# Kernel tuning notes

Measured on AMD Instinct MI355X. Metric: run time of the kernel, lower is better.

The kernel has to match this reference:

```python
import jax, jax.numpy as jnp
import numpy as np

B, N, D, H = 4, 2048, 1024, 16
DH = D // H

def setup_inputs() -> dict:
    key = jax.random.key(0)
    kx, kqkv, ko = jax.random.split(key, 3)
    x = jax.random.normal(kx, (B, N, D), dtype=jnp.float32)
    # torch Linear weights: [out, in]; scale like default init
    W_qkv = jax.random.normal(kqkv, (3 * D, D), dtype=jnp.float32) * (1.0 / np.sqrt(D))
    W_out = jax.random.normal(ko, (D, D), dtype=jnp.float32) * (1.0 / np.sqrt(D))
    return {"x": x, "W_qkv": W_qkv, "W_out": W_out}

def reference(x, W_qkv, W_out):
    Bk, Nk, C = x.shape
    qkv = jnp.einsum('bnc,oc->bno', x, W_qkv)  # [B,N,3D]
    qkv = qkv.reshape(Bk, Nk, 3, H, DH).transpose(2, 0, 3, 1, 4)  # [3,B,H,N,DH]
    q, k, v = qkv[0], qkv[1], qkv[2]
    att = jnp.einsum('bhnd,bhmd->bhnm', q, k) * (1.0 / np.sqrt(DH))
    mask = jnp.triu(jnp.ones((Nk, Nk), dtype=bool), k=1)  # True above diagonal
    att = jnp.where(mask, -jnp.inf, att)
    att = jax.nn.softmax(att, axis=-1)
    y = jnp.einsum('bhnm,bhmd->bhnd', att, v)  # [B,H,N,DH]
    y = y.transpose(0, 2, 1, 3).reshape(Bk, Nk, C)
    return jnp.einsum('bnc,oc->bno', y, W_out)
```

## Files before the change

### kernel.cpp

```cpp
#include <hip/hip_runtime.h>
#include <hip/hip_bf16.h>
#include <stdint.h>

#define Bb 4
#define Nn 2048
#define Dd 1024
#define Hh 16
#define DHd 64
#define Mm (Bb*Nn)
#define D3 (3*Dd)

typedef unsigned short u16;
typedef unsigned int u32;
typedef __attribute__((ext_vector_type(8))) short bf16x8;
typedef __attribute__((ext_vector_type(4))) float f32x4;
typedef __attribute__((ext_vector_type(2))) unsigned int u32x2;
typedef __attribute__((ext_vector_type(4))) unsigned int u32x4;

__device__ __forceinline__ u16 f2bf(float f) {
    unsigned int u = __float_as_uint(f);
    u = (u + 0x7FFFu + ((u >> 16) & 1u)) >> 16;
    return (u16)u;
}

__device__ __forceinline__ u32 cvtpk_bf16(float lo, float hi) {
    u32 r;
    asm("v_cvt_pk_bf16_f32 %0, %1, %2" : "=v"(r) : "v"(lo), "v"(hi));
    return r;
}

__device__ __forceinline__ float fexp2(float x) {
    float r;
    asm("v_exp_f32 %0, %1" : "=v"(r) : "v"(x));
    return r;
}

#define GLOAD16(g, l)                                                          \
    __builtin_amdgcn_global_load_lds(                                          \
        (const __attribute__((address_space(1))) unsigned int*)(g),            \
        (__attribute__((address_space(3))) unsigned int*)(l), 16, 0, 0)

__global__ void cvt_f32_bf16(const float* __restrict__ in, u16* __restrict__ out, int n4) {
    int i = blockIdx.x * blockDim.x + threadIdx.x;
    int stride = gridDim.x * blockDim.x;
    for (; i < n4; i += stride) {
        float4 v = ((const float4*)in)[i];
        u16 o0 = f2bf(v.x), o1 = f2bf(v.y), o2 = f2bf(v.z), o3 = f2bf(v.w);
        unsigned int lo = (unsigned int)o0 | ((unsigned int)o1 << 16);
        unsigned int hi = (unsigned int)o2 | ((unsigned int)o3 << 16);
        ((uint2*)out)[i] = make_uint2(lo, hi);
    }
}

__global__ void cvt_f32_bf16_s(const float* __restrict__ in, u16* __restrict__ out,
                               int n4, int cut4, float s) {
    int i = blockIdx.x * blockDim.x + threadIdx.x;
    int stride = gridDim.x * blockDim.x;
    for (; i < n4; i += stride) {
        float4 v = ((const float4*)in)[i];
        float sc = (i < cut4) ? s : 1.0f;
        u16 o0 = f2bf(v.x * sc), o1 = f2bf(v.y * sc), o2 = f2bf(v.z * sc), o3 = f2bf(v.w * sc);
        unsigned int lo = (unsigned int)o0 | ((unsigned int)o1 << 16);
        unsigned int hi = (unsigned int)o2 | ((unsigned int)o3 << 16);
        ((uint2*)out)[i] = make_uint2(lo, hi);
    }
}

template<int OUT_F32>
__global__ __launch_bounds__(256) void gemm_bt(const u16* __restrict__ A,
                                               const u16* __restrict__ Bm,
                                               void* __restrict__ C,
                                               int M, int Nout, int K) {
    __shared__ u16 As[128 * 64];
    __shared__ u16 Bs[128 * 64];
    const int t = threadIdx.x;
    const int lane = t & 63;
    const int w = t >> 6;
    const int wr = w >> 1, wc = w & 1;
    const int l15 = lane & 15, l4 = lane >> 4;
    const int m0 = blockIdx.y * 128;
    const int n0 = blockIdx.x * 128;

    f32x4 acc[4][4] = {};

    for (int k0 = 0; k0 < K; k0 += 64) {
        __syncthreads();
#pragma unroll
        for (int i = 0; i < 4; i++) {
            int chunk = i * 256 + t;
            int row = chunk >> 3;
            int csw = ((chunk & 7) ^ (row & 7)) << 3;
            GLOAD16(A + (size_t)(m0 + row) * K + k0 + csw, &As[chunk * 8]);
            GLOAD16(Bm + (size_t)(n0 + row) * K + k0 + csw, &Bs[chunk * 8]);
        }
        __syncthreads();

#pragma unroll
        for (int kh = 0; kh < 2; kh++) {
            bf16x8 a[4], b[4];
#pragma unroll
            for (int mi = 0; mi < 4; mi++) {
                int row = wr * 64 + mi * 16 + l15;
                a[mi] = *(const bf16x8*)&As[row * 64 + (((kh * 4 + l4) ^ (row & 7)) << 3)];
            }
#pragma unroll
            for (int nj = 0; nj < 4; nj++) {
                int row = wc * 64 + nj * 16 + l15;
                b[nj] = *(const bf16x8*)&Bs[row * 64 + (((kh * 4 + l4) ^ (row & 7)) << 3)];
            }
#pragma unroll
            for (int mi = 0; mi < 4; mi++)
#pragma unroll
                for (int nj = 0; nj < 4; nj++)
                    acc[mi][nj] = __builtin_amdgcn_mfma_f32_16x16x32_bf16(a[mi], b[nj], acc[mi][nj], 0, 0, 0);
        }
    }

#pragma unroll
    for (int mi = 0; mi < 4; mi++) {
#pragma unroll
        for (int nj = 0; nj < 4; nj++) {
            int col = n0 + wc * 64 + nj * 16 + l15;
#pragma unroll
            for (int r = 0; r < 4; r++) {
                int row = m0 + wr * 64 + mi * 16 + l4 * 4 + r;
                float v = acc[mi][nj][r];
                if (OUT_F32)
                    ((float*)C)[(size_t)row * Nout + col] = v;
                else
                    ((u16*)C)[(size_t)row * Nout + col] = f2bf(v);
            }
        }
    }
}

__global__ __launch_bounds__(512) void attn(const u16* __restrict__ qkv, u16* __restrict__ y) {
    __shared__ u16 Kt[2][64 * 64];
    __shared__ u16 Vt[2][64 * 64];

    const int t = threadIdx.x;
    const int lane = t & 63;
    const int w = t >> 6;
    const int l15 = lane & 15, l4 = lane >> 4;
    const int bh = blockIdx.x * 8 + (blockIdx.y & 7);
    const int pairidx = blockIdx.y >> 3;
    const int b = bh >> 4, h = bh & 15;

    const u16* qbase = qkv + (size_t)(b * Nn) * D3 + h * DHd;
    const u16* Kg = qbase + Dd;
    const u16* Vg = qbase + 2 * Dd;

    const int krow = t >> 3;
    const int ksw = (((t & 7) ^ (krow & 7)) << 3);
    const int vi = t & 31;
    const int vsd = (t >> 5) * 4;
    const int vchunk = (2 * vi) >> 3;
    const int vcol = (2 * vi) & 7;

    const bool hi2 = (lane >> 5) & 1;
    const bool bit0 = (lane >> 4) & 1;
    const int sgrp = lane & 48;

    bool mgt[4];
#pragma unroll
    for (int r = 0; r < 4; r++) mgt[r] = (l4 * 4 + r) > l15;

    for (int pass = 0; pass < 2; ++pass) {
        const int qt = pass == 0 ? pairidx : (15 - pairidx);
        const int q0 = qt * 128;
        const int ktmax = 2 * qt + 1;
        const int qwmin = q0 + w * 16;

        bf16x8 qf[2];
        {
            const u16* qrow = qbase + (size_t)(qwmin + l15) * D3;
            qf[0] = *(const bf16x8*)(qrow + l4 * 8);
            qf[1] = *(const bf16x8*)(qrow + 32 + l4 * 8);
        }

        f32x4 o[4] = {};
        float m_ = -1e30f;
        float l_ = 0.f;

        u32x2 va, vb_;

        GLOAD16(Kg + (size_t)krow * D3 + ksw, &Kt[0][t * 8]);
        {
            const u16* vr = Vg + (size_t)(2 * vi) * D3 + vsd;
            va = *(const u32x2*)vr;
            vb_ = *(const u32x2*)(vr + D3);
        }
        asm volatile("s_waitcnt vmcnt(0)" ::: "memory");
        {
            u16 av[4], bv[4];
            *(u32x2*)av = va; *(u32x2*)bv = vb_;
#pragma unroll
            for (int j = 0; j < 4; j++) {
                int d = vsd + j;
                u32 word = (u32)av[j] | ((u32)bv[j] << 16);
                *(u32*)&Vt[0][d * 64 + ((vchunk ^ (d & 7)) << 3) + vcol] = word;
            }
        }
        __syncthreads();

        int cur = 0;
        for (int kt = 0; kt <= ktmax; ++kt) {
            const int k0 = kt * 64;
            const int havenext = (kt < ktmax);

            if (havenext) {
                const int nk0 = k0 + 64;
                GLOAD16(Kg + (size_t)(nk0 + krow) * D3 + ksw, &Kt[cur ^ 1][t * 8]);
                const u16* vr = Vg + (size_t)(nk0 + 2 * vi) * D3 + vsd;
                va = *(const u32x2*)vr;
                vb_ = *(const u32x2*)(vr + D3);
            }

            const int dks = (qwmin - k0) >> 4;

            if (dks >= 0) {
                const int kcm = dks < 3 ? dks : 3;
                const int kgm = (dks >> 1) < 1 ? (dks >> 1) : 1;

                f32x4 sv[4];
                float vmax = -3.0e38f;
                __builtin_amdgcn_s_setprio(1);
#pragma unroll
                for (int kc = 0; kc < 4; ++kc) {
                    if (kc <= kcm) {
                        f32x4 s = {};
                        int row = kc * 16 + l15;
                        int sw = row & 7;
                        bf16x8 kf0 = *(const bf16x8*)&Kt[cur][row * 64 + ((l4 ^ sw) << 3)];
                        bf16x8 kf1 = *(const bf16x8*)&Kt[cur][row * 64 + (((4 + l4) ^ sw) << 3)];
                        s = __builtin_amdgcn_mfma_f32_16x16x32_bf16(kf0, qf[0], s, 0, 0, 0);
                        s = __builtin_amdgcn_mfma_f32_16x16x32_bf16(kf1, qf[1], s, 0, 0, 0);
                        const bool bmask = (kc == dks);
#pragma unroll
                        for (int r = 0; r < 4; r++) {
                            float x = s[r];
                            if (bmask && mgt[r]) x = -1e30f;
                            sv[kc][r] = x;
                            vmax = fmaxf(vmax, x);
                        }
                    }
                }
                __builtin_amdgcn_s_setprio(0);

                vmax = fmaxf(vmax, __shfl_xor(vmax, 16));
                vmax = fmaxf(vmax, __shfl_xor(vmax, 32));

                if (!__all(vmax <= m_ + 8.f)) {
                    float newm = fmaxf(m_, vmax);
                    float corr = fexp2(m_ - newm);
                    l_ *= corr;
                    float corr_o[4];
#pragma unroll
                    for (int r = 0; r < 4; ++r)
                        corr_o[r] = __shfl(corr, sgrp | (((lane >> 4) & 3) * 4 + r));
#pragma unroll
                    for (int db = 0; db < 4; db++)
#pragma unroll
                        for (int r = 0; r < 4; r++) o[db][r] *= corr_o[r];
                    m_ = newm;
                }

                u32 up[4][2];
#pragma unroll
                for (int kc = 0; kc < 4; ++kc) {
                    if (kc <= kcm) {
                        float p0 = fexp2(sv[kc][0] - m_);
                        float p1 = fexp2(sv[kc][1] - m_);
                        float p2 = fexp2(sv[kc][2] - m_);
                        float p3 = fexp2(sv[kc][3] - m_);
                        l_ += (p0 + p1) + (p2 + p3);
                        up[kc][0] = cvtpk_bf16(p0, p1);
                        up[kc][1] = cvtpk_bf16(p2, p3);
                    } else {
                        up[kc][0] = 0u;
                        up[kc][1] = 0u;
                    }
                }

                __builtin_amdgcn_s_setprio(1);
#pragma unroll
                for (int kg = 0; kg < 2; kg++) {
                    if (kg <= kgm) {
                        u32 paya0 = hi2 ? up[2 * kg + 1][0] : up[2 * kg][0];
                        u32 paya1 = hi2 ? up[2 * kg + 1][1] : up[2 * kg][1];
                        u32 payb0 = hi2 ? up[2 * kg][0] : up[2 * kg + 1][0];
                        u32 payb1 = hi2 ? up[2 * kg][1] : up[2 * kg + 1][1];
                        u32 a16_0 = (u32)__shfl_xor((int)paya0, 16);
                        u32 a16_1 = (u32)__shfl_xor((int)paya1, 16);
                        u32 a32_0 = (u32)__shfl_xor((int)payb0, 32);
                        u32 a32_1 = (u32)__shfl_xor((int)payb1, 32);
                        u32 a48_0 = (u32)__shfl_xor((int)payb0, 48);
                        u32 a48_1 = (u32)__shfl_xor((int)payb1, 48);
                        u32x4 tt;
                        tt[0] = hi2 ? (bit0 ? a16_0 : a32_0) : (bit0 ? a48_0 : paya0);
                        tt[1] = hi2 ? (bit0 ? a16_1 : a32_1) : (bit0 ? a48_1 : paya1);
                        tt[2] = hi2 ? (bit0 ? paya0 : a48_0) : (bit0 ? a32_0 : a16_0);
                        tt[3] = hi2 ? (bit0 ? paya1 : a48_1) : (bit0 ? a32_1 : a16_1);
                        union { u32x4 u; bf16x8 b; } pa;
                        pa.u = tt;
#pragma unroll
                        for (int db = 0; db < 4; db++) {
                            int d = db * 16 + l15;
                            bf16x8 vb = *(const bf16x8*)&Vt[cur][d * 64 + (((kg * 4 + l4) ^ (d & 7)) << 3)];
                            o[db] = __builtin_amdgcn_mfma_f32_16x16x32_bf16(pa.b, vb, o[db], 0, 0, 0);
                        }
                    }
                }
                __builtin_amdgcn_s_setprio(0);
            }

            if (havenext) {
                asm volatile("s_waitcnt vmcnt(0)" ::: "memory");
                u16 av[4], bv[4];
                *(u32x2*)av = va; *(u32x2*)bv = vb_;
#pragma unroll
                for (int j = 0; j < 4; j++) {
                    int d = vsd + j;
                    u32 word = (u32)av[j] | ((u32)bv[j] << 16);
                    *(u32*)&Vt[cur ^ 1][d * 64 + ((vchunk ^ (d & 7)) << 3) + vcol] = word;
                }
            }
            __syncthreads();
            cur ^= 1;
        }

        l_ += __shfl_xor(l_, 16);
        l_ += __shfl_xor(l_, 32);
        float linv = 1.f / l_;
        float linv_o[4];
#pragma unroll
        for (int r = 0; r < 4; ++r)
            linv_o[r] = __shfl(linv, sgrp | (((lane >> 4) & 3) * 4 + r));
#pragma unroll
        for (int r = 0; r < 4; r++) {
            int qg = qwmin + l4 * 4 + r;
            u16* yrow = y + (size_t)(b * Nn + qg) * Dd + h * DHd;
#pragma unroll
            for (int db = 0; db < 4; db++)
                yrow[db * 16 + l15] = f2bf(o[db][r] * linv_o[r]);
        }
    }
}

extern "C" void kernel_launch(void* const* d_in, const int* in_sizes, int n_in,
                              void* d_out, int out_size, void* d_ws, size_t ws_size,
                              hipStream_t stream) {
    const float* x = (const float*)d_in[0];
    const float* Wqkv = (const float*)d_in[1];
    const float* Wout = (const float*)d_in[2];

    char* ws = (char*)d_ws;
    size_t off = 0;
    u16* xb = (u16*)(ws + off);    off += (size_t)Mm * Dd * 2;
    u16* wqkvb = (u16*)(ws + off); off += (size_t)D3 * Dd * 2;
    u16* woutb = (u16*)(ws + off); off += (size_t)Dd * Dd * 2;
    u16* qkv = (u16*)(ws + off);   off += (size_t)Mm * D3 * 2;
    u16* yb = (u16*)(ws + off);    off += (size_t)Mm * Dd * 2;

    const float SCL = 0.125f * 1.4426950408889634f;

    cvt_f32_bf16<<<4096, 256, 0, stream>>>(x, xb, Mm * Dd / 4);
    cvt_f32_bf16_s<<<1024, 256, 0, stream>>>(Wqkv, wqkvb, D3 * Dd / 4, Dd * Dd / 4, SCL);
    cvt_f32_bf16<<<512, 256, 0, stream>>>(Wout, woutb, Dd * Dd / 4);

    gemm_bt<0><<<dim3(D3 / 128, Mm / 128), 256, 0, stream>>>(xb, wqkvb, qkv, Mm, D3, Dd);
    attn<<<dim3(Nn / 256, Bb * Hh), 512, 0, stream>>>(qkv, yb);
    gemm_bt<1><<<dim3(Dd / 128, Mm / 128), 256, 0, stream>>>(yb, woutb, d_out, Mm, Dd, Dd);
}
```

Baseline: 178.4 us.

## Split attention KV tiles across two wave groups and merge softmax partials in LDS

The attention block grows to 1024 threads, split into two groups of 8 waves. Each group processes alternating K/V tiles for the same query rows, giving a split-K flash-attention scheme whose partial max, sum and output are merged through shared memory at the end. Loading is also specialised: the first group issues K global-to-LDS loads and the second loads and transposes V. The aim is more parallelism per query tile. The cost is a larger LDS pool, register pressure from launch_bounds(1024,2), extra barriers and a merge step.

```diff
diff --git a/kernel.cpp b/kernel.cpp
--- a/kernel.cpp
+++ b/kernel.cpp
@@ -134,13 +134,19 @@
     }
 }
 
-__global__ __launch_bounds__(512) void attn(const u16* __restrict__ qkv, u16* __restrict__ y) {
-    __shared__ u16 Kt[2][64 * 64];
-    __shared__ u16 Vt[2][64 * 64];
+__global__ __launch_bounds__(1024, 2) void attn(const u16* __restrict__ qkv, u16* __restrict__ y) {
+    __shared__ __align__(16) char pool[35328];
+    u16 (*Kt)[4096] = reinterpret_cast<u16(*)[4096]>(pool);
+    u16 (*Vt)[4096] = reinterpret_cast<u16(*)[4096]>(pool + 16384);
+    float* MO = (float*)pool;
+    float* ML = (float*)(pool + 32768);
+    float* MM = (float*)(pool + 34816);
 
     const int t = threadIdx.x;
     const int lane = t & 63;
     const int w = t >> 6;
+    const int wl = w & 7;
+    const int par = w >> 3;
     const int l15 = lane & 15, l4 = lane >> 4;
     const int bh = blockIdx.x * 8 + (blockIdx.y & 7);
     const int pairidx = blockIdx.y >> 3;
@@ -152,8 +158,9 @@
 
     const int krow = t >> 3;
     const int ksw = (((t & 7) ^ (krow & 7)) << 3);
-    const int vi = t & 31;
-    const int vsd = (t >> 5) * 4;
+    const int tv = t & 511;
+    const int vi = tv & 31;
+    const int vsd = (tv >> 5) * 4;
     const int vchunk = (2 * vi) >> 3;
     const int vcol = (2 * vi) & 7;
 
@@ -169,7 +176,7 @@
         const int qt = pass == 0 ? pairidx : (15 - pairidx);
         const int q0 = qt * 128;
         const int ktmax = 2 * qt + 1;
-        const int qwmin = q0 + w * 16;
+        const int qwmin = q0 + wl * 16;
 
         bf16x8 qf[2];
         {
@@ -184,14 +191,13 @@
 
         u32x2 va, vb_;
 
-        GLOAD16(Kg + (size_t)krow * D3 + ksw, &Kt[0][t * 8]);
-        {
+        if (w < 8) {
+            GLOAD16(Kg + (size_t)krow * D3 + ksw, &Kt[0][t * 8]);
+        } else {
             const u16* vr = Vg + (size_t)(2 * vi) * D3 + vsd;
             va = *(const u32x2*)vr;
             vb_ = *(const u32x2*)(vr + D3);
-        }
-        asm volatile("s_waitcnt vmcnt(0)" ::: "memory");
-        {
+            asm volatile("s_waitcnt vmcnt(0)" ::: "memory");
             u16 av[4], bv[4];
             *(u32x2*)av = va; *(u32x2*)bv = vb_;
 #pragma unroll
@@ -210,15 +216,18 @@
 
             if (havenext) {
                 const int nk0 = k0 + 64;
-                GLOAD16(Kg + (size_t)(nk0 + krow) * D3 + ksw, &Kt[cur ^ 1][t * 8]);
-                const u16* vr = Vg + (size_t)(nk0 + 2 * vi) * D3 + vsd;
-                va = *(const u32x2*)vr;
-                vb_ = *(const u32x2*)(vr + D3);
+                if (w < 8) {
+                    GLOAD16(Kg + (size_t)(nk0 + krow) * D3 + ksw, &Kt[cur ^ 1][t * 8]);
+                } else {
+                    const u16* vr = Vg + (size_t)(nk0 + 2 * vi) * D3 + vsd;
+                    va = *(const u32x2*)vr;
+                    vb_ = *(const u32x2*)(vr + D3);
+                }
             }
 
             const int dks = (qwmin - k0) >> 4;
 
-            if (dks >= 0) {
+            if (((kt & 1) == par) && dks >= 0) {
                 const int kcm = dks < 3 ? dks : 3;
                 const int kgm = (dks >> 1) < 1 ? (dks >> 1) : 1;
 
@@ -314,7 +323,7 @@
                 __builtin_amdgcn_s_setprio(0);
             }
 
-            if (havenext) {
+            if (havenext && w >= 8) {
                 asm volatile("s_waitcnt vmcnt(0)" ::: "memory");
                 u16 av[4], bv[4];
                 *(u32x2*)av = va; *(u32x2*)bv = vb_;
@@ -329,21 +338,55 @@
             cur ^= 1;
         }
 
-        l_ += __shfl_xor(l_, 16);
-        l_ += __shfl_xor(l_, 32);
-        float linv = 1.f / l_;
-        float linv_o[4];
-#pragma unroll
-        for (int r = 0; r < 4; ++r)
-            linv_o[r] = __shfl(linv, sgrp | (((lane >> 4) & 3) * 4 + r));
-#pragma unroll
-        for (int r = 0; r < 4; r++) {
-            int qg = qwmin + l4 * 4 + r;
-            u16* yrow = y + (size_t)(b * Nn + qg) * Dd + h * DHd;
+        if (w >= 8) {
+            const int wu = w - 8;
+            if (lane < 16) MM[wu * 16 + lane] = m_;
+            ML[wu * 64 + lane] = l_;
+            float* mo = MO + wu * 1024 + lane * 16;
 #pragma unroll
             for (int db = 0; db < 4; db++)
-                yrow[db * 16 + l15] = f2bf(o[db][r] * linv_o[r]);
-        }
+                *(f32x4*)(mo + db * 4) = o[db];
+        }
+        __syncthreads();
+        if (w < 8) {
+            float mB = MM[wl * 16 + l15];
+            float M = fmaxf(m_, mB);
+            float ca = fexp2(m_ - M);
+            float cb = fexp2(mB - M);
+            l_ = l_ * ca + ML[wl * 64 + lane] * cb;
+            float ca_o[4], cb_o[4];
+#pragma unroll
+            for (int r = 0; r < 4; ++r) {
+                int src = sgrp | (((lane >> 4) & 3) * 4 + r);
+                ca_o[r] = __shfl(ca, src);
+                cb_o[r] = __shfl(cb, src);
+            }
+            const float* mo = MO + wl * 1024 + lane * 16;
+#pragma unroll
+            for (int db = 0; db < 4; db++) {
+                f32x4 ob = *(const f32x4*)(mo + db * 4);
+#pragma unroll
+                for (int r = 0; r < 4; r++)
+                    o[db][r] = o[db][r] * ca_o[r] + ob[r] * cb_o[r];
+            }
+
+            l_ += __shfl_xor(l_, 16);
+            l_ += __shfl_xor(l_, 32);
+            float linv = 1.f / l_;
+            float linv_o[4];
+#pragma unroll
+            for (int r = 0; r < 4; ++r)
+                linv_o[r] = __shfl(linv, sgrp | (((lane >> 4) & 3) * 4 + r));
+#pragma unroll
+            for (int r = 0; r < 4; r++) {
+                int qg = qwmin + l4 * 4 + r;
+                u16* yrow = y + (size_t)(b * Nn + qg) * Dd + h * DHd;
+#pragma unroll
+                for (int db = 0; db < 4; db++)
+                    yrow[db * 16 + l15] = f2bf(o[db][r] * linv_o[r]);
+            }
+        }
+        __syncthreads();
     }
 }
 
@@ -369,6 +412,6 @@
     cvt_f32_bf16<<<512, 256, 0, stream>>>(Wout, woutb, Dd * Dd / 4);
 
     gemm_bt<0><<<dim3(D3 / 128, Mm / 128), 256, 0, stream>>>(xb, wqkvb, qkv, Mm, D3, Dd);
-    attn<<<dim3(Nn / 256, Bb * Hh), 512, 0, stream>>>(qkv, yb);
+    attn<<<dim3(Nn / 256, Bb * Hh), 1024, 0, stream>>>(qkv, yb);
     gemm_bt<1><<<dim3(Dd / 128, Mm / 128), 256, 0, stream>>>(yb, woutb, d_out, Mm, Dd, Dd);
 }
```

Result: slower. 210.2 us (+17.8%).

## Shrink attention blocks to 64-row query tiles and swizzle GEMM tile order

Applied to the files above, without the earlier changes.

The attention kernel moves from 512-thread blocks handling 128-row query tiles to 256-thread blocks handling 64-row tiles. Each thread now loads twice as much K/V data, the grid grows to 8x128, and the diagonal-skip branch is removed because every warp now sees valid keys. The GEMM remaps block indices so groups of eight consecutive blocks land on strided tiles, aiming for better cache locality across XCDs. The goal is finer causal load balancing and higher occupancy, at the cost of more blocks reloading K/V overall.

```diff
diff --git a/kernel.cpp b/kernel.cpp
--- a/kernel.cpp
+++ b/kernel.cpp
@@ -14,7 +14,6 @@
 typedef unsigned int u32;
 typedef __attribute__((ext_vector_type(8))) short bf16x8;
 typedef __attribute__((ext_vector_type(4))) float f32x4;
-typedef __attribute__((ext_vector_type(2))) unsigned int u32x2;
 typedef __attribute__((ext_vector_type(4))) unsigned int u32x4;
 
 __device__ __forceinline__ u16 f2bf(float f) {
@@ -78,8 +77,13 @@
     const int w = t >> 6;
     const int wr = w >> 1, wc = w & 1;
     const int l15 = lane & 15, l4 = lane >> 4;
-    const int m0 = blockIdx.y * 128;
-    const int n0 = blockIdx.x * 128;
+
+    const int gx = gridDim.x;
+    const int linear = blockIdx.y * gx + blockIdx.x;
+    const int cpx = (gx * gridDim.y) >> 3;
+    const int tile = (linear & 7) * cpx + (linear >> 3);
+    const int m0 = (tile / gx) * 128;
+    const int n0 = (tile % gx) * 128;
 
     f32x4 acc[4][4] = {};
 
@@ -134,7 +138,7 @@
     }
 }
 
-__global__ __launch_bounds__(512) void attn(const u16* __restrict__ qkv, u16* __restrict__ y) {
+__global__ __launch_bounds__(256, 4) void attn(const u16* __restrict__ qkv, u16* __restrict__ y) {
     __shared__ u16 Kt[2][64 * 64];
     __shared__ u16 Vt[2][64 * 64];
 
@@ -153,7 +157,7 @@
     const int krow = t >> 3;
     const int ksw = (((t & 7) ^ (krow & 7)) << 3);
     const int vi = t & 31;
-    const int vsd = (t >> 5) * 4;
+    const int vsd = (t >> 5) * 8;
     const int vchunk = (2 * vi) >> 3;
     const int vcol = (2 * vi) & 7;
 
@@ -166,9 +170,9 @@
     for (int r = 0; r < 4; r++) mgt[r] = (l4 * 4 + r) > l15;
 
     for (int pass = 0; pass < 2; ++pass) {
-        const int qt = pass == 0 ? pairidx : (15 - pairidx);
-        const int q0 = qt * 128;
-        const int ktmax = 2 * qt + 1;
+        const int qt = pass == 0 ? pairidx : (31 - pairidx);
+        const int q0 = qt * 64;
+        const int ktmax = qt;
         const int qwmin = q0 + w * 16;
 
         bf16x8 qf[2];
@@ -182,20 +186,21 @@
         float m_ = -1e30f;
         float l_ = 0.f;
 
-        u32x2 va, vb_;
+        u32x4 va, vb_;
 
         GLOAD16(Kg + (size_t)krow * D3 + ksw, &Kt[0][t * 8]);
+        GLOAD16(Kg + (size_t)(krow + 32) * D3 + ksw, &Kt[0][(t + 256) * 8]);
         {
             const u16* vr = Vg + (size_t)(2 * vi) * D3 + vsd;
-            va = *(const u32x2*)vr;
-            vb_ = *(const u32x2*)(vr + D3);
+            va = *(const u32x4*)vr;
+            vb_ = *(const u32x4*)(vr + D3);
         }
         asm volatile("s_waitcnt vmcnt(0)" ::: "memory");
         {
-            u16 av[4], bv[4];
-            *(u32x2*)av = va; *(u32x2*)bv = vb_;
-#pragma unroll
-            for (int j = 0; j < 4; j++) {
+            u16 av[8], bv[8];
+            *(u32x4*)av = va; *(u32x4*)bv = vb_;
+#pragma unroll
+            for (int j = 0; j < 8; j++) {
                 int d = vsd + j;
                 u32 word = (u32)av[j] | ((u32)bv[j] << 16);
                 *(u32*)&Vt[0][d * 64 + ((vchunk ^ (d & 7)) << 3) + vcol] = word;
@@ -211,115 +216,113 @@
             if (havenext) {
                 const int nk0 = k0 + 64;
                 GLOAD16(Kg + (size_t)(nk0 + krow) * D3 + ksw, &Kt[cur ^ 1][t * 8]);
+                GLOAD16(Kg + (size_t)(nk0 + krow + 32) * D3 + ksw, &Kt[cur ^ 1][(t + 256) * 8]);
                 const u16* vr = Vg + (size_t)(nk0 + 2 * vi) * D3 + vsd;
-                va = *(const u32x2*)vr;
-                vb_ = *(const u32x2*)(vr + D3);
+                va = *(const u32x4*)vr;
+                vb_ = *(const u32x4*)(vr + D3);
             }
 
             const int dks = (qwmin - k0) >> 4;
-
-            if (dks >= 0) {
-                const int kcm = dks < 3 ? dks : 3;
-                const int kgm = (dks >> 1) < 1 ? (dks >> 1) : 1;
-
-                f32x4 sv[4];
-                float vmax = -3.0e38f;
-                __builtin_amdgcn_s_setprio(1);
-#pragma unroll
-                for (int kc = 0; kc < 4; ++kc) {
-                    if (kc <= kcm) {
-                        f32x4 s = {};
-                        int row = kc * 16 + l15;
-                        int sw = row & 7;
-                        bf16x8 kf0 = *(const bf16x8*)&Kt[cur][row * 64 + ((l4 ^ sw) << 3)];
-                        bf16x8 kf1 = *(const bf16x8*)&Kt[cur][row * 64 + (((4 + l4) ^ sw) << 3)];
-                        s = __builtin_amdgcn_mfma_f32_16x16x32_bf16(kf0, qf[0], s, 0, 0, 0);
-                        s = __builtin_amdgcn_mfma_f32_16x16x32_bf16(kf1, qf[1], s, 0, 0, 0);
-                        const bool bmask = (kc == dks);
-#pragma unroll
-                        for (int r = 0; r < 4; r++) {
-                            float x = s[r];
-                            if (bmask && mgt[r]) x = -1e30f;
-                            sv[kc][r] = x;
-                            vmax = fmaxf(vmax, x);
-                        }
+            const int kcm = dks < 3 ? dks : 3;
+            const int kgm = (dks >> 1) < 1 ? (dks >> 1) : 1;
+
+            f32x4 sv[4];
+            float vmax = -3.0e38f;
+            __builtin_amdgcn_s_setprio(1);
+#pragma unroll
+            for (int kc = 0; kc < 4; ++kc) {
+                if (kc <= kcm) {
+                    f32x4 s = {};
+                    int row = kc * 16 + l15;
+                    int sw = row & 7;
+                    bf16x8 kf0 = *(const bf16x8*)&Kt[cur][row * 64 + ((l4 ^ sw) << 3)];
+                    bf16x8 kf1 = *(const bf16x8*)&Kt[cur][row * 64 + (((4 + l4) ^ sw) << 3)];
+                    s = __builtin_amdgcn_mfma_f32_16x16x32_bf16(kf0, qf[0], s, 0, 0, 0);
+                    s = __builtin_amdgcn_mfma_f32_16x16x32_bf16(kf1, qf[1], s, 0, 0, 0);
+                    const bool bmask = (kc == dks);
+#pragma unroll
+                    for (int r = 0; r < 4; r++) {
+                        float x = s[r];
+                        if (bmask && mgt[r]) x = -1e30f;
+                        sv[kc][r] = x;
+                        vmax = fmaxf(vmax, x);
                     }
                 }
-                __builtin_amdgcn_s_setprio(0);
-
-                vmax = fmaxf(vmax, __shfl_xor(vmax, 16));
-                vmax = fmaxf(vmax, __shfl_xor(vmax, 32));
-
-                if (!__all(vmax <= m_ + 8.f)) {
-                    float newm = fmaxf(m_, vmax);
-                    float corr = fexp2(m_ - newm);
-                    l_ *= corr;
-                    float corr_o[4];
-#pragma unroll
-                    for (int r = 0; r < 4; ++r)
-                        corr_o[r] = __shfl(corr, sgrp | (((lane >> 4) & 3) * 4 + r));
-#pragma unroll
-                    for (int db = 0; db < 4; db++)
-#pragma unroll
-                        for (int r = 0; r < 4; r++) o[db][r] *= corr_o[r];
-                    m_ = newm;
+            }
+            __builtin_amdgcn_s_setprio(0);
+
+            vmax = fmaxf(vmax, __shfl_xor(vmax, 16));
+            vmax = fmaxf(vmax, __shfl_xor(vmax, 32));
+
+            if (!__all(vmax <= m_ + 8.f)) {
+                float newm = fmaxf(m_, vmax);
+                float corr = fexp2(m_ - newm);
+                l_ *= corr;
+                float corr_o[4];
+#pragma unroll
+                for (int r = 0; r < 4; ++r)
+                    corr_o[r] = __shfl(corr, sgrp | (((lane >> 4) & 3) * 4 + r));
+#pragma unroll
+                for (int db = 0; db < 4; db++)
+#pragma unroll
+                    for (int r = 0; r < 4; r++) o[db][r] *= corr_o[r];
+                m_ = newm;
+            }
+
+            u32 up[4][2];
+#pragma unroll
+            for (int kc = 0; kc < 4; ++kc) {
+                if (kc <= kcm) {
+                    float p0 = fexp2(sv[kc][0] - m_);
+                    float p1 = fexp2(sv[kc][1] - m_);
+                    float p2 = fexp2(sv[kc][2] - m_);
+                    float p3 = fexp2(sv[kc][3] - m_);
+                    l_ += (p0 + p1) + (p2 + p3);
+                    up[kc][0] = cvtpk_bf16(p0, p1);
+                    up[kc][1] = cvtpk_bf16(p2, p3);
+                } else {
+                    up[kc][0] = 0u;
+                    up[kc][1] = 0u;
                 }
-
-                u32 up[4][2];
-#pragma unroll
-                for (int kc = 0; kc < 4; ++kc) {
-                    if (kc <= kcm) {
-                        float p0 = fexp2(sv[kc][0] - m_);
-                        float p1 = fexp2(sv[kc][1] - m_);
-                        float p2 = fexp2(sv[kc][2] - m_);
-                        float p3 = fexp2(sv[kc][3] - m_);
-                        l_ += (p0 + p1) + (p2 + p3);
-                        up[kc][0] = cvtpk_bf16(p0, p1);
-                        up[kc][1] = cvtpk_bf16(p2, p3);
-                    } else {
-                        up[kc][0] = 0u;
-                        up[kc][1] = 0u;
+            }
+
+            __builtin_amdgcn_s_setprio(1);
+#pragma unroll
+            for (int kg = 0; kg < 2; kg++) {
+                if (kg <= kgm) {
+                    u32 paya0 = hi2 ? up[2 * kg + 1][0] : up[2 * kg][0];
+                    u32 paya1 = hi2 ? up[2 * kg + 1][1] : up[2 * kg][1];
+                    u32 payb0 = hi2 ? up[2 * kg][0] : up[2 * kg + 1][0];
+                    u32 payb1 = hi2 ? up[2 * kg][1] : up[2 * kg + 1][1];
+                    u32 a16_0 = (u32)__shfl_xor((int)paya0, 16);
+                    u32 a16_1 = (u32)__shfl_xor((int)paya1, 16);
+                    u32 a32_0 = (u32)__shfl_xor((int)payb0, 32);
+                    u32 a32_1 = (u32)__shfl_xor((int)payb1, 32);
+                    u32 a48_0 = (u32)__shfl_xor((int)payb0, 48);
+                    u32 a48_1 = (u32)__shfl_xor((int)payb1, 48);
+                    u32x4 tt;
+                    tt[0] = hi2 ? (bit0 ? a16_0 : a32_0) : (bit0 ? a48_0 : paya0);
+                    tt[1] = hi2 ? (bit0 ? a16_1 : a32_1) : (bit0 ? a48_1 : paya1);
+                    tt[2] = hi2 ? (bit0 ? paya0 : a48_0) : (bit0 ? a32_0 : a16_0);
+                    tt[3] = hi2 ? (bit0 ? paya1 : a48_1) : (bit0 ? a32_1 : a16_1);
+                    union { u32x4 u; bf16x8 b; } pa;
+                    pa.u = tt;
+#pragma unroll
+                    for (int db = 0; db < 4; db++) {
+                        int d = db * 16 + l15;
+                        bf16x8 vb = *(const bf16x8*)&Vt[cur][d * 64 + (((kg * 4 + l4) ^ (d & 7)) << 3)];
+                        o[db] = __builtin_amdgcn_mfma_f32_16x16x32_bf16(pa.b, vb, o[db], 0, 0, 0);
                     }
                 }
-
-                __builtin_amdgcn_s_setprio(1);
-#pragma unroll
-                for (int kg = 0; kg < 2; kg++) {
-                    if (kg <= kgm) {
-                        u32 paya0 = hi2 ? up[2 * kg + 1][0] : up[2 * kg][0];
-                        u32 paya1 = hi2 ? up[2 * kg + 1][1] : up[2 * kg][1];
-                        u32 payb0 = hi2 ? up[2 * kg][0] : up[2 * kg + 1][0];
-                        u32 payb1 = hi2 ? up[2 * kg][1] : up[2 * kg + 1][1];
-                        u32 a16_0 = (u32)__shfl_xor((int)paya0, 16);
-                        u32 a16_1 = (u32)__shfl_xor((int)paya1, 16);
-                        u32 a32_0 = (u32)__shfl_xor((int)payb0, 32);
-                        u32 a32_1 = (u32)__shfl_xor((int)payb1, 32);
-                        u32 a48_0 = (u32)__shfl_xor((int)payb0, 48);
-                        u32 a48_1 = (u32)__shfl_xor((int)payb1, 48);
-                        u32x4 tt;
-                        tt[0] = hi2 ? (bit0 ? a16_0 : a32_0) : (bit0 ? a48_0 : paya0);
-                        tt[1] = hi2 ? (bit0 ? a16_1 : a32_1) : (bit0 ? a48_1 : paya1);
-                        tt[2] = hi2 ? (bit0 ? paya0 : a48_0) : (bit0 ? a32_0 : a16_0);
-                        tt[3] = hi2 ? (bit0 ? paya1 : a48_1) : (bit0 ? a32_1 : a16_1);
-                        union { u32x4 u; bf16x8 b; } pa;
-                        pa.u = tt;
-#pragma unroll
-                        for (int db = 0; db < 4; db++) {
-                            int d = db * 16 + l15;
-                            bf16x8 vb = *(const bf16x8*)&Vt[cur][d * 64 + (((kg * 4 + l4) ^ (d & 7)) << 3)];
-                            o[db] = __builtin_amdgcn_mfma_f32_16x16x32_bf16(pa.b, vb, o[db], 0, 0, 0);
-                        }
-                    }
-                }
-                __builtin_amdgcn_s_setprio(0);
-            }
+            }
+            __builtin_amdgcn_s_setprio(0);
 
             if (havenext) {
                 asm volatile("s_waitcnt vmcnt(0)" ::: "memory");
-                u16 av[4], bv[4];
-                *(u32x2*)av = va; *(u32x2*)bv = vb_;
-#pragma unroll
-                for (int j = 0; j < 4; j++) {
+                u16 av[8], bv[8];
+                *(u32x4*)av = va; *(u32x4*)bv = vb_;
+#pragma unroll
+                for (int j = 0; j < 8; j++) {
                     int d = vsd + j;
                     u32 word = (u32)av[j] | ((u32)bv[j] << 16);
                     *(u32*)&Vt[cur ^ 1][d * 64 + ((vchunk ^ (d & 7)) << 3) + vcol] = word;
@@ -369,6 +372,6 @@
     cvt_f32_bf16<<<512, 256, 0, stream>>>(Wout, woutb, Dd * Dd / 4);
 
     gemm_bt<0><<<dim3(D3 / 128, Mm / 128), 256, 0, stream>>>(xb, wqkvb, qkv, Mm, D3, Dd);
-    attn<<<dim3(Nn / 256, Bb * Hh), 512, 0, stream>>>(qkv, yb);
+    attn<<<dim3(8, 128), 256, 0, stream>>>(qkv, yb);
     gemm_bt<1><<<dim3(Dd / 128, Mm / 128), 256, 0, stream>>>(yb, woutb, d_out, Mm, Dd, Dd);
 }
```

After: 189.7 us. 1.06x slower.
